# Kernel tuning notes

Measured on AMD Instinct MI355X. Metric: run time of the kernel, lower is better.

Reference implementation:

```python
import jax, jax.numpy as jnp
import numpy as np

B, S, D = 2, 2048, 512
H, K = 8, 64  # n_heads, dim_k (== dim_v per original code)


def setup_inputs() -> dict:
    key = jax.random.key(0)
    ks = jax.random.split(key, 11)
    s = 0.02
    return {
        "query": jax.random.normal(ks[0], (B, S, D), jnp.float32),
        "key": jax.random.normal(ks[1], (B, S, D), jnp.float32),
        "value": jax.random.normal(ks[2], (B, S, D), jnp.float32),
        # per-head Dense projections (keras Dense has bias by default)
        "Wq": jax.random.normal(ks[3], (H, D, K), jnp.float32) * s,
        "bq": jnp.zeros((H, K), jnp.float32),
        "Wk": jax.random.normal(ks[4], (H, D, K), jnp.float32) * s,
        "bk": jnp.zeros((H, K), jnp.float32),
        "Wv": jax.random.normal(ks[5], (H, D, K), jnp.float32) * s,
        "bv": jnp.zeros((H, K), jnp.float32),
        "Wo": jax.random.normal(ks[6], (H * K, D), jnp.float32) * s,
        "bo": jnp.zeros((D,), jnp.float32),
    }


def reference(query, key, value, Wq, bq, Wk, bk, Wv, bv, Wo, bo):
    # per-head linear projections, vectorized over heads: [B,H,S,K]
    q = jnp.einsum("bsd,hdk->bhsk", query, Wq) + bq[:, None, :]
    k = jnp.einsum("bsd,hdk->bhsk", key, Wk) + bk[:, None, :]
    v = jnp.einsum("bsd,hdk->bhsk", value, Wv) + bv[:, None, :]
    # scaled dot-product: scores [B,H,S,S]
    scores = jnp.einsum("bhsk,bhtk->bhst", q, k) / jnp.sqrt(jnp.float32(K))
    attn = jax.nn.softmax(scores, axis=-1)
    ctx = jnp.einsum("bhst,bhtk->bhsk", attn, v)  # [B,H,S,K]
    # concat heads -> [B,S,H*K], then output projection
    ctx = jnp.transpose(ctx, (0, 2, 1, 3)).reshape(B, S, H * K)
    return ctx @ Wo + bo
```

## Files before the change

kernel.cpp:

```cpp
#include <hip/hip_runtime.h>

#define B 2
#define S 2048
#define D 512
#define H 8
#define KD 64

typedef __bf16 bf16_t;
typedef __bf16 bf16x8 __attribute__((ext_vector_type(8)));
typedef __bf16 bf16x4 __attribute__((ext_vector_type(4)));
typedef float f32x4 __attribute__((ext_vector_type(4)));

#define QSCALE 0.1803368801111204f

__device__ __forceinline__ void async_copy16(const void* g, void* l) {
    __builtin_amdgcn_global_load_lds(
        (const __attribute__((address_space(1))) void*)g,
        (__attribute__((address_space(3))) void*)l, 16, 0, 0);
}

__device__ __forceinline__ float max3f(float a, float b, float c) {
    float d;
    asm("v_max3_f32 %0, %1, %2, %3" : "=v"(d) : "v"(a), "v"(b), "v"(c));
    return d;
}

__global__ __launch_bounds__(256) void prep_kernel(
    const float* __restrict__ Wq, const float* __restrict__ Wk,
    const float* __restrict__ Wv, const float* __restrict__ Wo,
    bf16_t* __restrict__ Wtq, bf16_t* __restrict__ Wtk,
    bf16_t* __restrict__ Wtv, bf16_t* __restrict__ WoT)
{
    __shared__ bf16_t tl[64][72];
    const int blk = blockIdx.x, t = threadIdx.x;

    const float* src; bf16_t* dstbase;
    int ld, r0, c0;
    if (blk < 192) {
        const int mat = blk >> 6, h = (blk & 63) >> 3, dt = blk & 7;
        const float* W = (mat == 0) ? Wq : (mat == 1) ? Wk : Wv;
        bf16_t* Wt = (mat == 0) ? Wtq : (mat == 1) ? Wtk : Wtv;
        src = W + (size_t)h * D * KD; dstbase = Wt + (size_t)h * KD * D;
        ld = KD; r0 = dt * 64; c0 = 0;
    } else {
        const int kt = (blk - 192) >> 3, nt = (blk - 192) & 7;
        src = Wo; dstbase = WoT;
        ld = D; r0 = kt * 64; c0 = nt * 64;
    }

    {
        const int r = t >> 2, cq = (t & 3) * 16;
        const float* sp = src + (size_t)(r0 + r) * ld + c0 + cq;
#pragma unroll
        for (int q = 0; q < 4; ++q) {
            const float4 f = *reinterpret_cast<const float4*>(sp + q * 4);
            tl[r][cq + q * 4 + 0] = (bf16_t)f.x; tl[r][cq + q * 4 + 1] = (bf16_t)f.y;
            tl[r][cq + q * 4 + 2] = (bf16_t)f.z; tl[r][cq + q * 4 + 3] = (bf16_t)f.w;
        }
    }
    __syncthreads();
    {
        const int cc = t >> 2, rq = (t & 3) * 16;
        bf16x8 o0, o1;
#pragma unroll
        for (int j = 0; j < 8; ++j) { o0[j] = tl[rq + j][cc]; o1[j] = tl[rq + 8 + j][cc]; }
        bf16_t* dp = dstbase + (size_t)(c0 + cc) * 512 + r0 + rq;
        *reinterpret_cast<bf16x8*>(dp) = o0;
        *reinterpret_cast<bf16x8*>(dp + 8) = o1;
    }
}

__global__ __launch_bounds__(256) void xcvt_kernel(
    const float* __restrict__ q, const float* __restrict__ k, const float* __restrict__ v,
    bf16_t* __restrict__ xq, bf16_t* __restrict__ xk, bf16_t* __restrict__ xv)
{
    const int mat = blockIdx.y;
    const float* src = (mat == 0) ? q : (mat == 1) ? k : v;
    bf16_t* dst = (mat == 0) ? xq : (mat == 1) ? xk : xv;
    const size_t i8 = ((size_t)blockIdx.x * 256 + threadIdx.x) * 8;
    const float4 f0 = *reinterpret_cast<const float4*>(src + i8);
    const float4 f1 = *reinterpret_cast<const float4*>(src + i8 + 4);
    bf16x8 o;
    o[0] = (bf16_t)f0.x; o[1] = (bf16_t)f0.y; o[2] = (bf16_t)f0.z; o[3] = (bf16_t)f0.w;
    o[4] = (bf16_t)f1.x; o[5] = (bf16_t)f1.y; o[6] = (bf16_t)f1.z; o[7] = (bf16_t)f1.w;
    *reinterpret_cast<bf16x8*>(dst + i8) = o;
}

__device__ __forceinline__ void gemm_tile(
    const bf16_t* __restrict__ A, const bf16_t* __restrict__ Bt,
    int row0, int n0, char* lds, f32x4 (&acc)[2][2])
{
    const int tid = threadIdx.x, wave = tid >> 6, lane = tid & 63;
    const int g = lane >> 4, c = lane & 15;

    const int srow8 = lane >> 3, sslot = lane & 7;
    const bf16_t* asrc[2]; const bf16_t* bsrc[2];
#pragma unroll
    for (int j = 0; j < 2; ++j) {
        const int r = wave * 16 + j * 8 + srow8;
        const int ys = (r & 7) ^ (((r >> 3) & 1) << 2);
        asrc[j] = A + (size_t)(row0 + r) * 512 + ((sslot ^ ys) << 3);
        bsrc[j] = Bt + (size_t)(n0 + r) * 512 + ((sslot ^ ys) << 3);
    }
    const int adst = wave * 2048;
    const int bdst = 8192 + wave * 2048;

    const int ysr = (c & 7) ^ (((c >> 3) & 1) << 2);
    const int wm = wave >> 1, wn = wave & 1;
    int ard[2], brd[2];
#pragma unroll
    for (int f = 0; f < 2; ++f) {
        ard[f] = (wm * 32 + f * 16 + c) * 128;
        brd[f] = 8192 + (wn * 32 + f * 16 + c) * 128;
    }

#define GSTAGE(bufi, kt)                                                       \
    do { char* bp = lds + (bufi) * 16384;                                      \
        _Pragma("unroll") for (int j = 0; j < 2; ++j) {                        \
            async_copy16(asrc[j] + (kt) * 64, bp + adst + j * 1024);           \
            async_copy16(bsrc[j] + (kt) * 64, bp + bdst + j * 1024);           \
        }                                                                      \
    } while (0)

    int buf = 0;
    GSTAGE(0, 0);
    __syncthreads();
#pragma unroll 1
    for (int kt = 0; kt < 8; ++kt) {
        if (kt < 7) GSTAGE(buf ^ 1, kt + 1);
        const char* bp = lds + buf * 16384;
        __builtin_amdgcn_s_setprio(1);
#pragma unroll
        for (int ksub = 0; ksub < 2; ++ksub) {
            const int so = (((ksub << 2) | g) ^ ysr) << 4;
            bf16x8 bfr[2];
#pragma unroll
            for (int nf = 0; nf < 2; ++nf)
                bfr[nf] = *reinterpret_cast<const bf16x8*>(bp + brd[nf] + so);
#pragma unroll
            for (int mf = 0; mf < 2; ++mf) {
                const bf16x8 afr = *reinterpret_cast<const bf16x8*>(bp + ard[mf] + so);
                acc[mf][0] = __builtin_amdgcn_mfma_f32_16x16x32_bf16(afr, bfr[0], acc[mf][0], 0, 0, 0);
                acc[mf][1] = __builtin_amdgcn_mfma_f32_16x16x32_bf16(afr, bfr[1], acc[mf][1], 0, 0, 0);
            }
        }
        __builtin_amdgcn_s_setprio(0);
        __syncthreads();
        buf ^= 1;
    }
#undef GSTAGE
}

__global__ __launch_bounds__(256) void qkv_kernel(
    const bf16_t* __restrict__ xq, const bf16_t* __restrict__ xk, const bf16_t* __restrict__ xv,
    const bf16_t* __restrict__ Wtq, const bf16_t* __restrict__ Wtk, const bf16_t* __restrict__ Wtv,
    const float* __restrict__ bq, const float* __restrict__ bk, const float* __restrict__ bv,
    bf16_t* __restrict__ Qo, bf16_t* __restrict__ Ko, bf16_t* __restrict__ VTo)
{
    __shared__ char lds[2][16384];

    const int mat = blockIdx.y;
    const bf16_t* A    = (mat == 0) ? xq  : (mat == 1) ? xk  : xv;
    const bf16_t* Bt   = (mat == 0) ? Wtq : (mat == 1) ? Wtk : Wtv;
    const float* bias  = (mat == 0) ? bq  : (mat == 1) ? bk  : bv;
    const float scale  = (mat == 0) ? QSCALE : 1.0f;

    const int mtile = blockIdx.x & 63;
    const int ntile = blockIdx.x >> 6;
    const int row0 = mtile * 64, n0 = ntile * 64;

    const int lane = threadIdx.x & 63;
    const int g = lane >> 4, c = lane & 15;
    const int wave = threadIdx.x >> 6, wm = wave >> 1, wn = wave & 1;

    const f32x4 zero = {0.f, 0.f, 0.f, 0.f};
    f32x4 acc[2][2] = {{zero, zero}, {zero, zero}};
    gemm_tile(A, Bt, row0, n0, &lds[0][0], acc);

#pragma unroll
    for (int mf = 0; mf < 2; ++mf)
#pragma unroll
        for (int nf = 0; nf < 2; ++nf) {
            const int n = n0 + wn * 32 + nf * 16 + c;
            const int h = n >> 6, col = n & 63;
            const float bval = bias[n];
            const int rowb = row0 + wm * 32 + mf * 16 + 4 * g;
            const int b = rowb >> 11, s0 = rowb & 2047;
            const int bh = b * H + h;
            if (mat < 2) {
                bf16_t* outp = (mat == 0) ? Qo : Ko;
#pragma unroll
                for (int i = 0; i < 4; ++i)
                    outp[((size_t)bh * S + s0 + i) * KD + col] =
                        (bf16_t)((acc[mf][nf][i] + bval) * scale);
            } else {
                bf16x4 o;
#pragma unroll
                for (int i = 0; i < 4; ++i) o[i] = (bf16_t)(acc[mf][nf][i] + bval);
                *reinterpret_cast<bf16x4*>(VTo + ((size_t)bh * KD + col) * S + s0) = o;
            }
        }
}

template <int SPLIT>
__global__ __launch_bounds__(512) void attn_kernel(
    const bf16_t* __restrict__ Q, const bf16_t* __restrict__ Km,
    const bf16_t* __restrict__ VT,
    bf16_t* __restrict__ CTX, bf16_t* __restrict__ Opart, float* __restrict__ ML)
{
    __shared__ char kv_lds[2][16384];

    const int hw = blockIdx.x;
    const int xcd = hw & 7;
    const int idx = hw >> 3;
    const int bh = xcd * 2 + (idx >= 16 * SPLIT ? 1 : 0);
    const int r2 = idx & (16 * SPLIT - 1);
    const int chunk = r2 >> 4;
    const int stile = r2 & 15;
    const int b = bh >> 3, h = bh & (H - 1);

    const int tid = threadIdx.x, wave = tid >> 6, lane = tid & 63;
    const int g = lane >> 4, c = lane & 15;
    const int q0 = stile * 128 + wave * 16;
    const int kvbeg = chunk * (S / SPLIT);
    const int NT = (S / SPLIT) / 64;

    const bf16_t* kg = Km + (size_t)bh * S * KD;
    const bf16_t* vg = VT + (size_t)bh * KD * S;

    const bf16_t* qp = Q + ((size_t)bh * S + q0 + c) * KD;
    const bf16x8 qlo = *reinterpret_cast<const bf16x8*>(qp + g * 8);
    const bf16x8 qhi = *reinterpret_cast<const bf16x8*>(qp + 32 + g * 8);

    bf16x8 ones;
#pragma unroll
    for (int i = 0; i < 8; ++i) ones[i] = (bf16_t)1.0f;

    int koff[4][2], voff[4][2];
#pragma unroll
    for (int tt = 0; tt < 4; ++tt) {
        const int row = 8 * (c >> 2) + (c & 3) + 4 * (tt & 1) + 32 * (tt >> 1);
        const int ys = (row & 7) ^ (((row >> 3) & 1) << 2);
        koff[tt][0] = row * 128 + ((g * 16) ^ (ys << 4));
        koff[tt][1] = row * 128 + ((64 + g * 16) ^ (ys << 4));
    }
#pragma unroll
    for (int ct = 0; ct < 4; ++ct) {
        const int row = ct * 16 + c;
        const int ys = (row & 7) ^ (((row >> 3) & 1) << 2);
        voff[ct][0] = 8192 + row * 128 + ((g * 16) ^ (ys << 4));
        voff[ct][1] = 8192 + row * 128 + ((64 + g * 16) ^ (ys << 4));
    }

    const int srow = lane >> 3, sslot = lane & 7;
    const int kwv = wave & 3;
    const int krow0a = kwv * 16, krow0b = kwv * 16 + 8;
    const int rowa = krow0a + srow, rowb = krow0b + srow;
    const int ysa = (rowa & 7) ^ (((rowa >> 3) & 1) << 2);
    const int ysb = (rowb & 7) ^ (((rowb >> 3) & 1) << 2);
    const int ssa = sslot ^ ysa, ssb = sslot ^ ysb;

    const f32x4 zero = {0.f, 0.f, 0.f, 0.f};
    f32x4 acc[4] = {zero, zero, zero, zero};
    f32x4 accl = zero;
    float m_run = -1e30f;

#define STAGE(bufidx, kv0)                                                        \
    do {                                                                          \
        char* bp = kv_lds[0] + (bufidx) * 16384;                                  \
        if (wave < 4) {                                                           \
            async_copy16(kg + (size_t)((kv0) + rowa) * KD + ssa * 8, bp + krow0a * 128); \
            async_copy16(kg + (size_t)((kv0) + rowb) * KD + ssb * 8, bp + krow0b * 128); \
        } else {                                                                  \
            async_copy16(vg + (size_t)rowa * S + (kv0) + ssa * 8, bp + 8192 + krow0a * 128); \
            async_copy16(vg + (size_t)rowb * S + (kv0) + ssb * 8, bp + 8192 + krow0b * 128); \
        }                                                                         \
    } while (0)

    STAGE(0, kvbeg);
    __syncthreads();

    int buf = 0;
    for (int t = 0; t < NT; ++t) {
        if (t < NT - 1) STAGE(buf ^ 1, kvbeg + (t + 1) * 64);
        const char* kb = kv_lds[0] + buf * 16384;

        f32x4 sc[4];
        __builtin_amdgcn_s_setprio(1);
#pragma unroll
        for (int tt = 0; tt < 4; ++tt) {
            const bf16x8 k0f = *reinterpret_cast<const bf16x8*>(kb + koff[tt][0]);
            const bf16x8 k1f = *reinterpret_cast<const bf16x8*>(kb + koff[tt][1]);
            f32x4 z = zero;
            z = __builtin_amdgcn_mfma_f32_16x16x32_bf16(k0f, qlo, z, 0, 0, 0);
            sc[tt] = __builtin_amdgcn_mfma_f32_16x16x32_bf16(k1f, qhi, z, 0, 0, 0);
        }
        __builtin_amdgcn_s_setprio(0);

        const float m0 = max3f(sc[0][0], sc[0][1], sc[0][2]);
        const float m1 = max3f(sc[0][3], sc[1][0], sc[1][1]);
        const float m2 = max3f(sc[1][2], sc[1][3], sc[2][0]);
        const float m3 = max3f(sc[2][1], sc[2][2], sc[2][3]);
        const float m4 = max3f(sc[3][0], sc[3][1], sc[3][2]);
        float pm = fmaxf(max3f(max3f(m0, m1, m2), m3, m4), sc[3][3]);
        if (!__all(pm <= m_run + 8.0f)) {
            pm = fmaxf(pm, __shfl_xor(pm, 16));
            pm = fmaxf(pm, __shfl_xor(pm, 32));
            const float mn = fmaxf(m_run, pm);
            const float fs = exp2f(m_run - mn);
            m_run = mn;
            accl = accl * fs;
#pragma unroll
            for (int ct = 0; ct < 4; ++ct) acc[ct] = acc[ct] * fs;
        }

        bf16x8 f0, f1;
#pragma unroll
        for (int i = 0; i < 4; ++i) {
            f0[i]     = (bf16_t)exp2f(sc[0][i] - m_run);
            f0[4 + i] = (bf16_t)exp2f(sc[1][i] - m_run);
            f1[i]     = (bf16_t)exp2f(sc[2][i] - m_run);
            f1[4 + i] = (bf16_t)exp2f(sc[3][i] - m_run);
        }

        __builtin_amdgcn_s_setprio(1);
        accl = __builtin_amdgcn_mfma_f32_16x16x32_bf16(ones, f0, accl, 0, 0, 0);
        accl = __builtin_amdgcn_mfma_f32_16x16x32_bf16(ones, f1, accl, 0, 0, 0);
#pragma unroll
        for (int ct = 0; ct < 4; ++ct) {
            const bf16x8 v0f = *reinterpret_cast<const bf16x8*>(kb + voff[ct][0]);
            const bf16x8 v1f = *reinterpret_cast<const bf16x8*>(kb + voff[ct][1]);
            acc[ct] = __builtin_amdgcn_mfma_f32_16x16x32_bf16(v0f, f0, acc[ct], 0, 0, 0);
            acc[ct] = __builtin_amdgcn_mfma_f32_16x16x32_bf16(v1f, f1, acc[ct], 0, 0, 0);
        }
        __builtin_amdgcn_s_setprio(0);

        __syncthreads();
        buf ^= 1;
    }
#undef STAGE

    const float l_tot = accl[0];

    if constexpr (SPLIT == 1) {
        const float inv = 1.0f / l_tot;
        bf16_t* crow = CTX + ((size_t)b * S + q0 + c) * 512 + h * 64;
#pragma unroll
        for (int ct = 0; ct < 4; ++ct) {
            bf16x4 o;
#pragma unroll
            for (int i = 0; i < 4; ++i) o[i] = (bf16_t)(acc[ct][i] * inv);
            *reinterpret_cast<bf16x4*>(crow + ct * 16 + 4 * g) = o;
        }
    } else {
        const size_t prow = (size_t)(chunk * 16 + bh) * 2048 + q0 + c;
        bf16_t* orow = Opart + prow * 64;
#pragma unroll
        for (int ct = 0; ct < 4; ++ct) {
            bf16x4 o;
#pragma unroll
            for (int i = 0; i < 4; ++i) o[i] = (bf16_t)acc[ct][i];
            *reinterpret_cast<bf16x4*>(orow + ct * 16 + 4 * g) = o;
        }
        if (g == 0) {
            float2 ml; ml.x = m_run; ml.y = l_tot;
            *reinterpret_cast<float2*>(ML + prow * 2) = ml;
        }
    }
}

template <int SPLIT>
__global__ __launch_bounds__(256) void combine_kernel(
    const bf16_t* __restrict__ Opart, const float* __restrict__ ML,
    bf16_t* __restrict__ CTX)
{
    const int gid = blockIdx.x * 256 + threadIdx.x;
    const int d4 = gid & 15, rowh = gid >> 4;
    const int bh = rowh >> 11, s = rowh & 2047;
    const int b = bh >> 3, h = bh & (H - 1);

    float m[SPLIT], l[SPLIT], M = -1e30f;
#pragma unroll
    for (int i = 0; i < SPLIT; ++i) {
        const float2 v = *reinterpret_cast<const float2*>(
            ML + ((size_t)(i * 16 + bh) * 2048 + s) * 2);
        m[i] = v.x; l[i] = v.y;
        M = fmaxf(M, m[i]);
    }
    f32x4 o = {0.f, 0.f, 0.f, 0.f};
    float wsum = 0.f;
#pragma unroll
    for (int i = 0; i < SPLIT; ++i) {
        const float w = exp2f(m[i] - M);
        wsum += w * l[i];
        const bf16x4 ov = *reinterpret_cast<const bf16x4*>(
            Opart + ((size_t)(i * 16 + bh) * 2048 + s) * 64 + d4 * 4);
#pragma unroll
        for (int j = 0; j < 4; ++j) o[j] += w * (float)ov[j];
    }
    const float inv = 1.0f / wsum;
    bf16x4 r;
#pragma unroll
    for (int i = 0; i < 4; ++i) r[i] = (bf16_t)(o[i] * inv);
    *reinterpret_cast<bf16x4*>(CTX + ((size_t)b * S + s) * 512 + h * 64 + d4 * 4) = r;
}

__global__ __launch_bounds__(256) void out_proj_kernel(
    const bf16_t* __restrict__ CTX,
    const bf16_t* __restrict__ WoT,
    const float* __restrict__ bo,
    float* __restrict__ out)
{
    __shared__ char lds[2][16384];

    const int mtile = blockIdx.x & 63;
    const int ntile = blockIdx.x >> 6;
    const int row0 = mtile * 64, n0 = ntile * 64;

    const int lane = threadIdx.x & 63;
    const int g = lane >> 4, c = lane & 15;
    const int wave = threadIdx.x >> 6, wm = wave >> 1, wn = wave & 1;

    const f32x4 zero = {0.f, 0.f, 0.f, 0.f};
    f32x4 acc[2][2] = {{zero, zero}, {zero, zero}};
    gemm_tile(CTX, WoT, row0, n0, &lds[0][0], acc);

#pragma unroll
    for (int mf = 0; mf < 2; ++mf)
#pragma unroll
        for (int nf = 0; nf < 2; ++nf) {
            const int n = n0 + wn * 32 + nf * 16 + c;
            const float bval = bo[n];
            const int rowb = row0 + wm * 32 + mf * 16 + 4 * g;
#pragma unroll
            for (int i = 0; i < 4; ++i)
                out[(size_t)(rowb + i) * 512 + n] = acc[mf][nf][i] + bval;
        }
}

extern "C" void kernel_launch(void* const* d_in, const int* in_sizes, int n_in,
                              void* d_out, int out_size, void* d_ws, size_t ws_size,
                              hipStream_t stream) {
    const float* query = (const float*)d_in[0];
    const float* key_  = (const float*)d_in[1];
    const float* value = (const float*)d_in[2];
    const float* Wq = (const float*)d_in[3];
    const float* bq = (const float*)d_in[4];
    const float* Wk = (const float*)d_in[5];
    const float* bk = (const float*)d_in[6];
    const float* Wv = (const float*)d_in[7];
    const float* bv = (const float*)d_in[8];
    const float* Wo = (const float*)d_in[9];
    const float* bo = (const float*)d_in[10];

    char* wsb = (char*)d_ws;
    bf16_t* Qw   = (bf16_t*)(wsb);
    bf16_t* Kw   = (bf16_t*)(wsb + (4u  << 20));
    bf16_t* VTw  = (bf16_t*)(wsb + (8u  << 20));
    bf16_t* CTXb = (bf16_t*)(wsb + (12u << 20));
    bf16_t* Wtq  = (bf16_t*)(wsb + (16u << 20));
    bf16_t* Wtk  = Wtq + 8 * 64 * 512;
    bf16_t* Wtv  = Wtk + 8 * 64 * 512;
    bf16_t* WoTw = (bf16_t*)(wsb + (18u << 20));
    bf16_t* Xq   = (bf16_t*)(wsb + (20u << 20));
    bf16_t* Xk   = (bf16_t*)(wsb + (24u << 20));
    bf16_t* Xv   = (bf16_t*)(wsb + (28u << 20));
    bf16_t* Opart = (bf16_t*)(wsb + (32u << 20));

    const int SPLIT = (ws_size >= (70ull << 20)) ? 4
                    : (ws_size >= (52ull << 20)) ? 2 : 1;

    prep_kernel<<<256, 256, 0, stream>>>(Wq, Wk, Wv, Wo, Wtq, Wtk, Wtv, WoTw);
    xcvt_kernel<<<dim3(1024, 3), 256, 0, stream>>>(query, key_, value, Xq, Xk, Xv);
    qkv_kernel<<<dim3(512, 3), 256, 0, stream>>>(Xq, Xk, Xv,
                                                 Wtq, Wtk, Wtv, bq, bk, bv,
                                                 Qw, Kw, VTw);

    if (SPLIT == 4) {
        float* MLp = (float*)(Opart + 4ull * 16 * 2048 * 64);
        attn_kernel<4><<<1024, 512, 0, stream>>>(Qw, Kw, VTw, CTXb, Opart, MLp);
        combine_kernel<4><<<2048, 256, 0, stream>>>(Opart, MLp, CTXb);
    } else if (SPLIT == 2) {
        float* MLp = (float*)(Opart + 2ull * 16 * 2048 * 64);
        attn_kernel<2><<<512, 512, 0, stream>>>(Qw, Kw, VTw, CTXb, Opart, MLp);
        combine_kernel<2><<<2048, 256, 0, stream>>>(Opart, MLp, CTXb);
    } else {
        attn_kernel<1><<<256, 512, 0, stream>>>(Qw, Kw, VTw, CTXb, nullptr, nullptr);
    }

    out_proj_kernel<<<512, 256, 0, stream>>>(CTXb, WoTw, bo, (float*)d_out);
}
```

Before: 76.12 us.

## Switch attention kernel to 32x32x16 MFMA with 4 waves of 32 query rows

```diff
diff --git a/kernel.cpp b/kernel.cpp
--- a/kernel.cpp
+++ b/kernel.cpp
@@ -10,6 +10,7 @@
 typedef __bf16 bf16x8 __attribute__((ext_vector_type(8)));
 typedef __bf16 bf16x4 __attribute__((ext_vector_type(4)));
 typedef float f32x4 __attribute__((ext_vector_type(4)));
+typedef float f32x16 __attribute__((ext_vector_type(16)));
 
 #define QSCALE 0.1803368801111204f
 
@@ -203,7 +204,7 @@
 }
 
 template <int SPLIT>
-__global__ __launch_bounds__(512) void attn_kernel(
+__global__ __launch_bounds__(256) void attn_kernel(
     const bf16_t* __restrict__ Q, const bf16_t* __restrict__ Km,
     const bf16_t* __restrict__ VT,
     bf16_t* __restrict__ CTX, bf16_t* __restrict__ Opart, float* __restrict__ ML)
@@ -217,65 +218,69 @@
     const int r2 = idx & (16 * SPLIT - 1);
     const int chunk = r2 >> 4;
     const int stile = r2 & 15;
-    const int b = bh >> 3, h = bh & (H - 1);
+    const int b = bh >> 3, hh = bh & (H - 1);
 
     const int tid = threadIdx.x, wave = tid >> 6, lane = tid & 63;
-    const int g = lane >> 4, c = lane & 15;
-    const int q0 = stile * 128 + wave * 16;
+    const int q = lane & 31, lh = lane >> 5;
+    const int q0w = stile * 128 + wave * 32;
     const int kvbeg = chunk * (S / SPLIT);
     const int NT = (S / SPLIT) / 64;
 
     const bf16_t* kg = Km + (size_t)bh * S * KD;
     const bf16_t* vg = VT + (size_t)bh * KD * S;
 
-    const bf16_t* qp = Q + ((size_t)bh * S + q0 + c) * KD;
-    const bf16x8 qlo = *reinterpret_cast<const bf16x8*>(qp + g * 8);
-    const bf16x8 qhi = *reinterpret_cast<const bf16x8*>(qp + 32 + g * 8);
-
-    bf16x8 ones;
-#pragma unroll
-    for (int i = 0; i < 8; ++i) ones[i] = (bf16_t)1.0f;
-
-    int koff[4][2], voff[4][2];
-#pragma unroll
-    for (int tt = 0; tt < 4; ++tt) {
-        const int row = 8 * (c >> 2) + (c & 3) + 4 * (tt & 1) + 32 * (tt >> 1);
-        const int ys = (row & 7) ^ (((row >> 3) & 1) << 2);
-        koff[tt][0] = row * 128 + ((g * 16) ^ (ys << 4));
-        koff[tt][1] = row * 128 + ((64 + g * 16) ^ (ys << 4));
-    }
-#pragma unroll
-    for (int ct = 0; ct < 4; ++ct) {
-        const int row = ct * 16 + c;
-        const int ys = (row & 7) ^ (((row >> 3) & 1) << 2);
-        voff[ct][0] = 8192 + row * 128 + ((g * 16) ^ (ys << 4));
-        voff[ct][1] = 8192 + row * 128 + ((64 + g * 16) ^ (ys << 4));
-    }
-
-    const int srow = lane >> 3, sslot = lane & 7;
-    const int kwv = wave & 3;
-    const int krow0a = kwv * 16, krow0b = kwv * 16 + 8;
-    const int rowa = krow0a + srow, rowb = krow0b + srow;
-    const int ysa = (rowa & 7) ^ (((rowa >> 3) & 1) << 2);
-    const int ysb = (rowb & 7) ^ (((rowb >> 3) & 1) << 2);
-    const int ssa = sslot ^ ysa, ssb = sslot ^ ysb;
-
-    const f32x4 zero = {0.f, 0.f, 0.f, 0.f};
-    f32x4 acc[4] = {zero, zero, zero, zero};
-    f32x4 accl = zero;
-    float m_run = -1e30f;
-
-#define STAGE(bufidx, kv0)                                                        \
-    do {                                                                          \
-        char* bp = kv_lds[0] + (bufidx) * 16384;                                  \
-        if (wave < 4) {                                                           \
-            async_copy16(kg + (size_t)((kv0) + rowa) * KD + ssa * 8, bp + krow0a * 128); \
-            async_copy16(kg + (size_t)((kv0) + rowb) * KD + ssb * 8, bp + krow0b * 128); \
-        } else {                                                                  \
-            async_copy16(vg + (size_t)rowa * S + (kv0) + ssa * 8, bp + 8192 + krow0a * 128); \
-            async_copy16(vg + (size_t)rowb * S + (kv0) + ssb * 8, bp + 8192 + krow0b * 128); \
-        }                                                                         \
+    bf16x8 qf[4];
+    {
+        const bf16_t* qp = Q + ((size_t)bh * S + q0w + q) * KD + lh * 8;
+#pragma unroll
+        for (int ks = 0; ks < 4; ++ks) qf[ks] = *reinterpret_cast<const bf16x8*>(qp + ks * 16);
+    }
+
+    int koff[2][4], voff[2][4];
+    {
+        const int ysr = (q & 7) ^ (((q >> 3) & 1) << 2);
+#pragma unroll
+        for (int ks = 0; ks < 4; ++ks) {
+            const int xo = (ks * 32 + lh * 16) ^ (ysr << 4);
+            koff[0][ks] = q * 128 + xo;
+            koff[1][ks] = (q + 32) * 128 + xo;
+            voff[0][ks] = 8192 + q * 128 + xo;
+            voff[1][ks] = 8192 + (q + 32) * 128 + xo;
+        }
+    }
+
+    int ksrc[4]; size_t vsrc[4];
+    int kdst0, vdst0;
+    {
+        const int sr = lane >> 3, sl = lane & 7;
+        const int wlow = wave & 1;
+#pragma unroll
+        for (int j = 0; j < 4; ++j) {
+            const int a  = wlow * 32 + j * 8 + sr;
+            const int sa = (a & ~12) | ((a & 4) << 1) | ((a & 8) >> 1);
+            const int ys = (a & 7) ^ (((a >> 3) & 1) << 2);
+            ksrc[j] = sa * KD + (sl ^ ys) * 8;
+            vsrc[j] = (size_t)a * S + (sl ^ ys) * 8;
+        }
+        kdst0 = wlow * 4096;
+        vdst0 = 8192 + wlow * 4096;
+    }
+
+#define STAGE(bufidx, kv0)                                                     \
+    do {                                                                       \
+        char* bp = kv_lds[bufidx];                                             \
+        if (wave < 2) {                                                        \
+            _Pragma("unroll") for (int j = 0; j < 4; ++j)                      \
+                async_copy16(kg + (size_t)(kv0) * KD + ksrc[j],                \
+                             bp + kdst0 + j * 1024);                           \
+        } else {                                                               \
+            _Pragma("unroll") for (int j = 0; j < 4; ++j)                      \
+                async_copy16(vg + vsrc[j] + (kv0), bp + vdst0 + j * 1024);     \
+        }                                                                      \
     } while (0)
+
+    f32x16 o0 = {0.f}, o1 = {0.f};
+    float m_run = -1e30f, lsum = 0.f;
 
     STAGE(0, kvbeg);
     __syncthreads();
@@ -283,55 +288,73 @@
     int buf = 0;
     for (int t = 0; t < NT; ++t) {
         if (t < NT - 1) STAGE(buf ^ 1, kvbeg + (t + 1) * 64);
-        const char* kb = kv_lds[0] + buf * 16384;
-
-        f32x4 sc[4];
+        const char* kb = kv_lds[buf];
+
+        f32x16 sc0 = {0.f}, sc1 = {0.f};
         __builtin_amdgcn_s_setprio(1);
 #pragma unroll
-        for (int tt = 0; tt < 4; ++tt) {
-            const bf16x8 k0f = *reinterpret_cast<const bf16x8*>(kb + koff[tt][0]);
-            const bf16x8 k1f = *reinterpret_cast<const bf16x8*>(kb + koff[tt][1]);
-            f32x4 z = zero;
-            z = __builtin_amdgcn_mfma_f32_16x16x32_bf16(k0f, qlo, z, 0, 0, 0);
-            sc[tt] = __builtin_amdgcn_mfma_f32_16x16x32_bf16(k1f, qhi, z, 0, 0, 0);
+        for (int ks = 0; ks < 4; ++ks) {
+            const bf16x8 k0 = *reinterpret_cast<const bf16x8*>(kb + koff[0][ks]);
+            sc0 = __builtin_amdgcn_mfma_f32_32x32x16_bf16(k0, qf[ks], sc0, 0, 0, 0);
+            const bf16x8 k1 = *reinterpret_cast<const bf16x8*>(kb + koff[1][ks]);
+            sc1 = __builtin_amdgcn_mfma_f32_32x32x16_bf16(k1, qf[ks], sc1, 0, 0, 0);
         }
         __builtin_amdgcn_s_setprio(0);
 
-        const float m0 = max3f(sc[0][0], sc[0][1], sc[0][2]);
-        const float m1 = max3f(sc[0][3], sc[1][0], sc[1][1]);
-        const float m2 = max3f(sc[1][2], sc[1][3], sc[2][0]);
-        const float m3 = max3f(sc[2][1], sc[2][2], sc[2][3]);
-        const float m4 = max3f(sc[3][0], sc[3][1], sc[3][2]);
-        float pm = fmaxf(max3f(max3f(m0, m1, m2), m3, m4), sc[3][3]);
+        const float m0 = max3f(sc0[0],  sc0[1],  sc0[2]);
+        const float m1 = max3f(sc0[3],  sc0[4],  sc0[5]);
+        const float m2 = max3f(sc0[6],  sc0[7],  sc0[8]);
+        const float m3 = max3f(sc0[9],  sc0[10], sc0[11]);
+        const float m4 = max3f(sc0[12], sc0[13], sc0[14]);
+        const float m5 = max3f(sc0[15], sc1[0],  sc1[1]);
+        const float m6 = max3f(sc1[2],  sc1[3],  sc1[4]);
+        const float m7 = max3f(sc1[5],  sc1[6],  sc1[7]);
+        const float m8 = max3f(sc1[8],  sc1[9],  sc1[10]);
+        const float m9 = max3f(sc1[11], sc1[12], sc1[13]);
+        const float ma = fmaxf(sc1[14], sc1[15]);
+        const float mb = max3f(max3f(m0, m1, m2), max3f(m3, m4, m5), max3f(m6, m7, m8));
+        float pm = max3f(mb, max3f(m9, ma, -1e30f), -1e30f);
         if (!__all(pm <= m_run + 8.0f)) {
-            pm = fmaxf(pm, __shfl_xor(pm, 16));
             pm = fmaxf(pm, __shfl_xor(pm, 32));
             const float mn = fmaxf(m_run, pm);
             const float fs = exp2f(m_run - mn);
             m_run = mn;
-            accl = accl * fs;
-#pragma unroll
-            for (int ct = 0; ct < 4; ++ct) acc[ct] = acc[ct] * fs;
-        }
-
-        bf16x8 f0, f1;
-#pragma unroll
-        for (int i = 0; i < 4; ++i) {
-            f0[i]     = (bf16_t)exp2f(sc[0][i] - m_run);
-            f0[4 + i] = (bf16_t)exp2f(sc[1][i] - m_run);
-            f1[i]     = (bf16_t)exp2f(sc[2][i] - m_run);
-            f1[4 + i] = (bf16_t)exp2f(sc[3][i] - m_run);
-        }
+            lsum *= fs;
+            o0 *= fs; o1 *= fs;
+        }
+
+        bf16x8 pf0, pf1, pf2, pf3;
+        float ls = 0.f;
+#pragma unroll
+        for (int j = 0; j < 8; ++j) {
+            const float e0 = exp2f(sc0[j]     - m_run);
+            const float e1 = exp2f(sc0[8 + j] - m_run);
+            const float e2 = exp2f(sc1[j]     - m_run);
+            const float e3 = exp2f(sc1[8 + j] - m_run);
+            pf0[j] = (bf16_t)e0; pf1[j] = (bf16_t)e1;
+            pf2[j] = (bf16_t)e2; pf3[j] = (bf16_t)e3;
+            ls += (e0 + e1) + (e2 + e3);
+        }
+        lsum += ls;
 
         __builtin_amdgcn_s_setprio(1);
-        accl = __builtin_amdgcn_mfma_f32_16x16x32_bf16(ones, f0, accl, 0, 0, 0);
-        accl = __builtin_amdgcn_mfma_f32_16x16x32_bf16(ones, f1, accl, 0, 0, 0);
-#pragma unroll
-        for (int ct = 0; ct < 4; ++ct) {
-            const bf16x8 v0f = *reinterpret_cast<const bf16x8*>(kb + voff[ct][0]);
-            const bf16x8 v1f = *reinterpret_cast<const bf16x8*>(kb + voff[ct][1]);
-            acc[ct] = __builtin_amdgcn_mfma_f32_16x16x32_bf16(v0f, f0, acc[ct], 0, 0, 0);
-            acc[ct] = __builtin_amdgcn_mfma_f32_16x16x32_bf16(v1f, f1, acc[ct], 0, 0, 0);
+        {
+            const bf16x8 v00 = *reinterpret_cast<const bf16x8*>(kb + voff[0][0]);
+            const bf16x8 v10 = *reinterpret_cast<const bf16x8*>(kb + voff[1][0]);
+            o0 = __builtin_amdgcn_mfma_f32_32x32x16_bf16(v00, pf0, o0, 0, 0, 0);
+            o1 = __builtin_amdgcn_mfma_f32_32x32x16_bf16(v10, pf0, o1, 0, 0, 0);
+            const bf16x8 v01 = *reinterpret_cast<const bf16x8*>(kb + voff[0][1]);
+            const bf16x8 v11 = *reinterpret_cast<const bf16x8*>(kb + voff[1][1]);
+            o0 = __builtin_amdgcn_mfma_f32_32x32x16_bf16(v01, pf1, o0, 0, 0, 0);
+            o1 = __builtin_amdgcn_mfma_f32_32x32x16_bf16(v11, pf1, o1, 0, 0, 0);
+            const bf16x8 v02 = *reinterpret_cast<const bf16x8*>(kb + voff[0][2]);
+            const bf16x8 v12 = *reinterpret_cast<const bf16x8*>(kb + voff[1][2]);
+            o0 = __builtin_amdgcn_mfma_f32_32x32x16_bf16(v02, pf2, o0, 0, 0, 0);
+            o1 = __builtin_amdgcn_mfma_f32_32x32x16_bf16(v12, pf2, o1, 0, 0, 0);
+            const bf16x8 v03 = *reinterpret_cast<const bf16x8*>(kb + voff[0][3]);
+            const bf16x8 v13 = *reinterpret_cast<const bf16x8*>(kb + voff[1][3]);
+            o0 = __builtin_amdgcn_mfma_f32_32x32x16_bf16(v03, pf3, o0, 0, 0, 0);
+            o1 = __builtin_amdgcn_mfma_f32_32x32x16_bf16(v13, pf3, o1, 0, 0, 0);
         }
         __builtin_amdgcn_s_setprio(0);
 
@@ -340,30 +363,38 @@
     }
 #undef STAGE
 
-    const float l_tot = accl[0];
+    lsum += __shfl_xor(lsum, 32);
 
     if constexpr (SPLIT == 1) {
-        const float inv = 1.0f / l_tot;
-        bf16_t* crow = CTX + ((size_t)b * S + q0 + c) * 512 + h * 64;
-#pragma unroll
-        for (int ct = 0; ct < 4; ++ct) {
-            bf16x4 o;
-#pragma unroll
-            for (int i = 0; i < 4; ++i) o[i] = (bf16_t)(acc[ct][i] * inv);
-            *reinterpret_cast<bf16x4*>(crow + ct * 16 + 4 * g) = o;
+        const float inv = 1.0f / lsum;
+        bf16_t* crow = CTX + ((size_t)b * S + q0w + q) * 512 + hh * 64;
+#pragma unroll
+        for (int dg = 0; dg < 2; ++dg) {
+            const f32x16& o = dg ? o1 : o0;
+#pragma unroll
+            for (int quad = 0; quad < 4; ++quad) {
+                bf16x4 ov;
+#pragma unroll
+                for (int i = 0; i < 4; ++i) ov[i] = (bf16_t)(o[quad * 4 + i] * inv);
+                *reinterpret_cast<bf16x4*>(crow + dg * 32 + quad * 8 + lh * 4) = ov;
+            }
         }
     } else {
-        const size_t prow = (size_t)(chunk * 16 + bh) * 2048 + q0 + c;
+        const size_t prow = (size_t)(chunk * 16 + bh) * 2048 + q0w + q;
         bf16_t* orow = Opart + prow * 64;
 #pragma unroll
-        for (int ct = 0; ct < 4; ++ct) {
-            bf16x4 o;
-#pragma unroll
-            for (int i = 0; i < 4; ++i) o[i] = (bf16_t)acc[ct][i];
-            *reinterpret_cast<bf16x4*>(orow + ct * 16 + 4 * g) = o;
-        }
-        if (g == 0) {
-            float2 ml; ml.x = m_run; ml.y = l_tot;
+        for (int dg = 0; dg < 2; ++dg) {
+            const f32x16& o = dg ? o1 : o0;
+#pragma unroll
+            for (int quad = 0; quad < 4; ++quad) {
+                bf16x4 ov;
+#pragma unroll
+                for (int i = 0; i < 4; ++i) ov[i] = (bf16_t)o[quad * 4 + i];
+                *reinterpret_cast<bf16x4*>(orow + dg * 32 + quad * 8 + lh * 4) = ov;
+            }
+        }
+        if (lh == 0) {
+            float2 ml; ml.x = m_run; ml.y = lsum;
             *reinterpret_cast<float2*>(ML + prow * 2) = ml;
         }
     }
@@ -478,14 +509,14 @@
 
     if (SPLIT == 4) {
         float* MLp = (float*)(Opart + 4ull * 16 * 2048 * 64);
-        attn_kernel<4><<<1024, 512, 0, stream>>>(Qw, Kw, VTw, CTXb, Opart, MLp);
+        attn_kernel<4><<<1024, 256, 0, stream>>>(Qw, Kw, VTw, CTXb, Opart, MLp);
         combine_kernel<4><<<2048, 256, 0, stream>>>(Opart, MLp, CTXb);
     } else if (SPLIT == 2) {
         float* MLp = (float*)(Opart + 2ull * 16 * 2048 * 64);
-        attn_kernel<2><<<512, 512, 0, stream>>>(Qw, Kw, VTw, CTXb, Opart, MLp);
+        attn_kernel<2><<<512, 256, 0, stream>>>(Qw, Kw, VTw, CTXb, Opart, MLp);
         combine_kernel<2><<<2048, 256, 0, stream>>>(Opart, MLp, CTXb);
     } else {
-        attn_kernel<1><<<256, 512, 0, stream>>>(Qw, Kw, VTw, CTXb, nullptr, nullptr);
+        attn_kernel<1><<<256, 256, 0, stream>>>(Qw, Kw, VTw, CTXb, nullptr, nullptr);
     }
 
     out_proj_kernel<<<512, 256, 0, stream>>>(CTXb, WoTw, bo, (float*)d_out);
```

Result: slower. 81.33 us (+6.8%).
